# Kernel optimization log

Measured on AMD Instinct MI355X. Metric: run time of the kernel, lower is better.

## Reference

```python
import jax, jax.numpy as jnp
import numpy as np

B, NB, V1, V2, S, J, D, F = 32, 10, 3, 3, 2, 25, 3, 8
DIN = D * F          # 24
H1, H2 = 2 * DIN, 3 * DIN  # 48, 72
NFEAT, NCLASS = 256, 60
EPS = 1e-5


def _layernorm(h, g, b):
    m = jnp.mean(h, axis=-1, keepdims=True)
    v = jnp.mean(jnp.square(h - m), axis=-1, keepdims=True)
    return (h - m) * jax.lax.rsqrt(v + EPS) * g + b


def setup_inputs() -> dict:
    key = jax.random.key(0)
    ks = jax.random.split(key, 12)
    x = jax.random.normal(ks[0], (B, NB, V1, V2, S * J, D, F), dtype=jnp.float32)
    a = jax.random.uniform(ks[1], (J, J), dtype=jnp.float32)
    adj = a / jnp.sum(a, axis=1, keepdims=True)  # row-normalized dense adjacency
    sc = 0.05
    return {
        "x": x,
        "adj": adj,
        "W1": sc * jax.random.normal(ks[2], (DIN, H1), jnp.float32),
        "b1": jnp.zeros((H1,), jnp.float32),
        "g1": jnp.ones((H1,), jnp.float32),
        "be1": jnp.zeros((H1,), jnp.float32),
        "W2": sc * jax.random.normal(ks[3], (H1, H2), jnp.float32),
        "b2": jnp.zeros((H2,), jnp.float32),
        "g2": jnp.ones((H2,), jnp.float32),
        "be2": jnp.zeros((H2,), jnp.float32),
        "W3": sc * jax.random.normal(ks[4], (H2, NFEAT), jnp.float32),
        "b3": jnp.zeros((NFEAT,), jnp.float32),
        "g3": jnp.ones((NFEAT,), jnp.float32),
        "be3": jnp.zeros((NFEAT,), jnp.float32),
        "Wc": sc * jax.random.normal(ks[5], (J * NFEAT, NCLASS), jnp.float32),
        "bc": jnp.zeros((NCLASS,), jnp.float32),
        "batch_size": B,
        "degree": 4,
        "nclass": NCLASS,
        "alpha": 0.2,
    }


def _sgc_precompute(f0, adj, degree, alpha):
    # f0: [..., J, NFEAT]; repeated sparse-style propagation with accumulation
    def step(carry, _):
        f, acc = carry
        f = jnp.einsum('ij,...jf->...if', adj, f)
        acc = acc + (1.0 - alpha) * f + alpha * f0
        return (f, acc), None
    (_, acc), _ = jax.lax.scan(step, (f0, jnp.zeros_like(f0)), None, length=degree)
    return acc / degree


def reference(x, adj, W1, b1, g1, be1, W2, b2, g2, be2, W3, b3, g3, be3,
              Wc, bc, batch_size, degree, nclass, alpha):
    # split joints into (subject, joint) and flatten (D, F) per joint -> [B,NB,V1,V2,S,J,DIN]
    h = x.reshape(B, NB, V1, V2, S, J, DIN)
    h = jax.nn.relu(_layernorm(h @ W1 + b1, g1, be1))
    h = jax.nn.relu(_layernorm(h @ W2 + b2, g2, be2))
    h = _layernorm(h @ W3 + b3, g3, be3)            # dropout is identity in eval
    h = _sgc_precompute(h, adj, degree, alpha)       # [B,NB,V1,V2,S,J,NFEAT]
    vec = h.reshape(B, NB, V1, V2, S, J * NFEAT)
    logits = vec @ Wc + bc                            # [B,NB,V1,V2,S,NCLASS]
    block_mean = jnp.mean(logits, axis=4)             # mean over subjects
    pred = jnp.mean(block_mean, axis=(1, 2, 3))       # [B, NCLASS]
    return block_mean, pred
```

## Files before the change

### kernel.cpp

```cpp
#include <hip/hip_runtime.h>
#include <hip/hip_bf16.h>

typedef __hip_bfloat16 bf16t;
typedef _Float16 half_t;
typedef __attribute__((ext_vector_type(2))) _Float16 half2v;
typedef __attribute__((ext_vector_type(8))) _Float16 half8v;
typedef __attribute__((ext_vector_type(4))) float f32x4;
typedef unsigned int uint32;

#define BB   32
#define NC   60
#define NROW 2880
#define NFOLDB 1600
#define EPSF 1e-5f
#define ALPHA 0.2f
#define DEG  4

#define WS_M_OFF    256
#define WS_PW_OFF   4096
#define WS_W3BF_OFF 28672
#define WS_W2BF_OFF 77824
#define WS_W1BF_OFF 88064
#define WS_WCP_OFF  101376
#define WS_WCPF_OFF 869376
#define WS_PART_OFF 1688576
#define WS_GH3_OFF  7586816
#define WS_NEED     44450816ULL

#define P_W1  0
#define P_B1  1152
#define P_G1  1200
#define P_BE1 1248
#define P_W2  1296
#define P_B2  4752
#define P_G2  4824
#define P_BE2 4896
#define P_B3  4968
#define P_G3  5224
#define P_BE3 5480
#define P_BC  5736
#define P_TOT 5796
#define R_W3E (P_TOT+24576)
#define R_W2E (R_W3E+5120)
#define R_W1E (R_W2E+1536)
#define PREP_K1B 145

#define LB_H3L 0
#define LB_A1  12800
#define LB_CS  12800
#define LB_A2  22016
#define LB_H3H 22016
#define LB_STW 35328
#define LB_ST2 37376
#define LDS_FTOT 9472

__device__ __forceinline__ float ldin(const void* p, int i, int isbf){
  return isbf ? __bfloat162float(((const bf16t*)p)[i]) : ((const float*)p)[i];
}
__device__ __forceinline__ void stout(void* p, int i, int isbf, float v){
  if(isbf) ((bf16t*)p)[i] = __float2bfloat16(v);
  else     ((float*)p)[i] = v;
}
__device__ __forceinline__ half2v u2h2(uint32 u){
  half2v h; __builtin_memcpy(&h,&u,4); return h;
}
__device__ __forceinline__ uint32 pk2u(float a, float b){
  auto r = __builtin_amdgcn_cvt_pkrtz(a, b);
  uint32 u; __builtin_memcpy(&u,&r,4); return u;
}


__global__ void k_prep(const void* W1,const void* b1,const void* g1,const void* be1,
                       const void* W2,const void* b2,const void* g2,const void* be2,
                       const void* W3,const void* b3,const void* g3,const void* be3,
                       const void* bc, const void* x, const void* adj,
                       int* flagp, float* pw, float* M,
                       half_t* W3bf, half_t* W2bf, half_t* W1bf){
  __shared__ float A[625], Pp[625], Q[625], Ss[625];
  __shared__ int cnt;
  int t = threadIdx.x, bid = blockIdx.x;
  if(t==0) cnt = 0;
  __syncthreads();
  {
    const unsigned short* xb = (const unsigned short*)x;
    unsigned short u = xb[2*t];
    int e = (u>>7)&0xFF;
    if(e>=100 && e<=141) atomicAdd(&cnt,1);
  }
  __syncthreads();
  int isbf = (cnt>=160) ? 1 : 0;
  if(bid==0 && t==0) flagp[0] = isbf;

  if(bid < PREP_K1B){
    int o = bid*256 + t;
    if(o < P_TOT){
      const void* src; int loc;
      if      (o < P_B1 ) { src=W1;  loc=o;        }
      else if (o < P_G1 ) { src=b1;  loc=o-P_B1;   }
      else if (o < P_BE1) { src=g1;  loc=o-P_G1;   }
      else if (o < P_W2 ) { src=be1; loc=o-P_BE1;  }
      else if (o < P_B2 ) { src=W2;  loc=o-P_W2;   }
      else if (o < P_G2 ) { src=b2;  loc=o-P_B2;   }
      else if (o < P_BE2) { src=g2;  loc=o-P_G2;   }
      else if (o < P_B3 ) { src=be2; loc=o-P_BE2;  }
      else if (o < P_G3 ) { src=b3;  loc=o-P_B3;   }
      else if (o < P_BE3) { src=g3;  loc=o-P_G3;   }
      else if (o < P_BC ) { src=be3; loc=o-P_BE3;  }
      else                { src=bc;  loc=o-P_BC;   }
      pw[o] = ldin(src, loc, isbf);
    } else if(o < R_W3E){
      int o2 = o - P_TOT;
      int ct = o2/1536, rem = o2 - ct*1536;
      int kt = rem/512, rem2 = rem - kt*512;
      int l = rem2>>3, j = rem2&7;
      int k = kt*32 + ((l>>4)<<3) + j;
      int col = (ct<<4) + (l&15);
      float v = (k<72) ? ldin(W3, k*256+col, isbf) : 0.f;
      W3bf[o2] = (half_t)v;
    } else if(o < R_W2E){
      int o2 = o - R_W3E;
      int ct = o2/1024, rem = o2 - ct*1024;
      int kt = rem/512, rem2 = rem - kt*512;
      int l = rem2>>3, j = rem2&7;
      int k = kt*32 + ((l>>4)<<3) + j;
      int col = (ct<<4) + (l&15);
      float v = (k<48 && col<72) ? ldin(W2, k*72+col, isbf) : 0.f;
      W2bf[o2] = (half_t)v;
    } else if(o < R_W1E){
      int o2 = o - R_W2E;
      int ct = o2/512, rem2 = o2 - ct*512;
      int l = rem2>>3, j = rem2&7;
      int k = ((l>>4)<<3) + j;
      int col = (ct<<4) + (l&15);
      float v = (k<24) ? ldin(W1, k*48+col, isbf) : 0.f;
      W1bf[o2] = (half_t)v;
    }
  } else {
    for(int i=t;i<625;i+=256){ float a=ldin(adj,i,isbf); A[i]=a; Pp[i]=a; Ss[i]=a; }
    __syncthreads();
    for(int d=1; d<DEG; ++d){
      for(int o=t;o<625;o+=256){
        int i=o/25, j=o%25; float acc=0.f;
        for(int k=0;k<25;k++) acc += A[i*25+k]*Pp[k*25+j];
        Q[o]=acc;
      }
      __syncthreads();
      for(int o=t;o<625;o+=256){ Pp[o]=Q[o]; Ss[o]+=Q[o]; }
      __syncthreads();
    }
    const float coef = (1.0f-ALPHA)/(float)DEG;
    for(int o=t;o<625;o+=256){
      int i=o/25, j=o%25;
      M[o] = (i==j ? ALPHA : 0.0f) + coef*Ss[o];
    }
  }
}

__global__ __launch_bounds__(256,4) void k3_fast(const void* x, const float* pw,
                                              const half_t* W3bf_, const half_t* W2bf_,
                                              const half_t* W1bf_,
                                              const float* M, const void* Wc,
                                              half_t* Wcpf,
                                              const int* flagp, uint32* gH3d){
  __shared__ float sm[LDS_FTOT];
  char* smb = (char*)sm;
  half_t* H3L = (half_t*)(smb + LB_H3L);
  half_t* H3H = (half_t*)(smb + LB_H3H);
  half_t* A1h = (half_t*)(smb + LB_A1);
  half_t* A2h = (half_t*)(smb + LB_A2);
  half_t* XH  = A2h;
  float*  stw = (float*)(smb + LB_STW);
  float*  st2 = (float*)(smb + LB_ST2);
  uint32* A1w = (uint32*)A1h;
  const unsigned short* W3u = (const unsigned short*)W3bf_;
  const unsigned short* W2u = (const unsigned short*)W2bf_;
  const unsigned short* W1u = (const unsigned short*)W1bf_;

  int t = threadIdx.x, bid = blockIdx.x;
  int isbf = flagp[0];

  if(bid >= NROW){
    int o = (bid-NROW)*256 + t;
    int j = o&7, l = (o>>3)&63, nt = (o>>9)&3, kst = o>>11;
    int k = kst*32 + ((l>>4)<<3) + j;
    int c = nt*16 + (l&15);
    float acc = 0.f;
    if(c < 60){
      int jj = k>>8, f = k&255;
      for(int i=0;i<25;i++) acc += M[i*25+jj]*ldin(Wc, (i*256+f)*60 + c, isbf);
    }
    Wcpf[o] = (half_t)(0.5f*acc);
    return;
  }

  int l = t&63, w = t>>6, cb = l&15, g4 = l>>4;
  const float* b1=pw+P_B1;  const float* g1=pw+P_G1;  const float* be1=pw+P_BE1;
  const float* b2=pw+P_B2;  const float* g2=pw+P_G2;  const float* be2=pw+P_BE2;
  const float* b3=pw+P_B3;  const float* g3=pw+P_G3;  const float* be3=pw+P_BE3;

  for(int o=t;o<512;o+=256){ int r=o>>3, dc=24+(o&7); A1w[r*36+dc]=0; }
  {
    int xoff = bid*1200;
    for(int i=t;i<2560;i+=256){
      int r=i/40, c=i-(i/40)*40;
      float v = (r<50 && c<24) ? ldin(x, xoff + r*24+c, isbf) : 0.f;
      XH[i] = (half_t)v;
    }
  }
  __syncthreads();

  {
    f32x4 acc1[3];
    float g1v[3], be1v[3];
    #pragma unroll
    for(int ct=0;ct<3;ct++){
      int col = ct*16 + cb;
      float b = b1[col]; g1v[ct]=g1[col]; be1v[ct]=be1[col];
      acc1[ct][0]=b; acc1[ct][1]=b; acc1[ct][2]=b; acc1[ct][3]=b;
    }
    half8v a = *(const half8v*)(XH + (w*16 + cb)*40 + (g4<<3));
    #pragma unroll
    for(int ct=0;ct<3;ct++){
      half8v b = *(const half8v*)(W1u + (ct*64 + l)*8);
      acc1[ct] = __builtin_amdgcn_mfma_f32_16x16x32_f16(a, b, acc1[ct], 0,0,0);
    }
    __syncthreads();
    #pragma unroll
    for(int r=0;r<4;r++){
      float s1 = acc1[0][r]+acc1[1][r]+acc1[2][r];
      float s2 = acc1[0][r]*acc1[0][r]+acc1[1][r]*acc1[1][r]+acc1[2][r]*acc1[2][r];
      #pragma unroll
      for(int d=1;d<16;d<<=1){ s1+=__shfl_xor(s1,d,64); s2+=__shfl_xor(s2,d,64); }
      float m = s1*(1.f/48.f);
      float var = s2*(1.f/48.f)-m*m;
      float rs = rsqrtf(var+EPSF);
      int row = w*16 + (g4<<2) + r;
      #pragma unroll
      for(int ct=0;ct<3;ct++){
        float val = (acc1[ct][r]-m)*rs*g1v[ct]+be1v[ct];
        A1h[row*72 + ct*16 + cb] = (half_t)fmaxf(val,0.f);
      }
    }
  }
  __syncthreads();

  {
    f32x4 acc2[5];
    #pragma unroll
    for(int ct=0;ct<5;ct++){
      int col = ct*16 + cb;
      float b = (col<72) ? b2[col] : 0.f;
      acc2[ct][0]=b; acc2[ct][1]=b; acc2[ct][2]=b; acc2[ct][3]=b;
    }
    #pragma unroll
    for(int kt=0;kt<2;kt++){
      half8v a = *(const half8v*)(A1h + (w*16 + cb)*72 + kt*32 + (g4<<3));
      #pragma unroll
      for(int ct=0;ct<5;ct++){
        half8v b = *(const half8v*)(W2u + ((ct*2+kt)*64 + l)*8);
        acc2[ct] = __builtin_amdgcn_mfma_f32_16x16x32_f16(a, b, acc2[ct], 0,0,0);
      }
    }
    __syncthreads();
    int valid4 = (cb<8);
    #pragma unroll
    for(int r=0;r<4;r++){
      float s1 = acc2[0][r]+acc2[1][r]+acc2[2][r]+acc2[3][r] + (valid4?acc2[4][r]:0.f);
      float s2 = acc2[0][r]*acc2[0][r]+acc2[1][r]*acc2[1][r]
               + acc2[2][r]*acc2[2][r]+acc2[3][r]*acc2[3][r]
               + (valid4?acc2[4][r]*acc2[4][r]:0.f);
      #pragma unroll
      for(int d=1;d<16;d<<=1){ s1+=__shfl_xor(s1,d,64); s2+=__shfl_xor(s2,d,64); }
      float m = s1*(1.f/72.f);
      float var = s2*(1.f/72.f)-m*m;
      float rs = rsqrtf(var+EPSF);
      int grow = w*16 + (g4<<2) + r;
      #pragma unroll
      for(int ct=0;ct<5;ct++){
        int col = ct*16 + cb;
        if(ct<4 || valid4){
          float val = (acc2[ct][r]-m)*rs*g2[col]+be2[col];
          A2h[grow*104+col] = (half_t)fmaxf(val,0.f);
        }
      }
    }
    uint32* A2w = (uint32*)A2h;
    for(int o=l;o<192;o+=64){ int rr = w*16 + o/12, dc = 36 + (o - (o/12)*12); A2w[rr*52+dc]=0; }
  }
  __syncthreads();

  #pragma unroll 1
  for(int p=0;p<2;p++){
    f32x4 acc[2][4];
    #pragma unroll
    for(int nt=0;nt<4;nt++){
      float b3c = b3[w*64 + nt*16 + cb];
      #pragma unroll
      for(int m2=0;m2<2;m2++){ acc[m2][nt][0]=b3c; acc[m2][nt][1]=b3c; acc[m2][nt][2]=b3c; acc[m2][nt][3]=b3c; }
    }
    #pragma unroll
    for(int kt=0;kt<3;kt++){
      half8v a[2];
      #pragma unroll
      for(int m2=0;m2<2;m2++)
        a[m2] = *(const half8v*)(A2h + ((p*2+m2)*16+cb)*104 + kt*32 + (g4<<3));
      #pragma unroll
      for(int nt=0;nt<4;nt++){
        int ct = w*4 + nt;
        half8v b = *(const half8v*)(W3u + ((ct*3+kt)*64 + l)*8);
        #pragma unroll
        for(int m2=0;m2<2;m2++)
          acc[m2][nt] = __builtin_amdgcn_mfma_f32_16x16x32_f16(a[m2], b, acc[m2][nt], 0,0,0);
      }
    }
    __syncthreads();
    #pragma unroll
    for(int m2=0;m2<2;m2++){
      #pragma unroll
      for(int r=0;r<4;r++){
        int row = (p*2+m2)*16 + (g4<<2) + r;
        float s1 = acc[m2][0][r]+acc[m2][1][r]+acc[m2][2][r]+acc[m2][3][r];
        float s2 = acc[m2][0][r]*acc[m2][0][r]+acc[m2][1][r]*acc[m2][1][r]
                 + acc[m2][2][r]*acc[m2][2][r]+acc[m2][3][r]*acc[m2][3][r];
        #pragma unroll
        for(int d=1;d<16;d<<=1){ s1+=__shfl_xor(s1,d,64); s2+=__shfl_xor(s2,d,64); }
        if(cb==0){
          stw[row*8 + w*2]   = s1;
          stw[row*8 + w*2+1] = s2;
        }
        if(row<50){
          #pragma unroll
          for(int nt=0;nt<4;nt++){
            int col = w*64 + nt*16 + cb;
            if(row<25) H3L[row*256+col]      = (half_t)acc[m2][nt][r];
            else       H3H[(row-25)*256+col] = (half_t)acc[m2][nt][r];
          }
        }
      }
    }
  }
  __syncthreads();
  if(t<64){
    float S1 = stw[t*8+0]+stw[t*8+2]+stw[t*8+4]+stw[t*8+6];
    float S2 = stw[t*8+1]+stw[t*8+3]+stw[t*8+5]+stw[t*8+7];
    float m = S1*(1.f/256.f);
    float var = S2*(1.f/256.f)-m*m;
    st2[2*t]=m; st2[2*t+1]=rsqrtf(var+EPSF);
  }
  __syncthreads();
  {
    uint32* H3l32 = (uint32*)H3L;
    uint32* H3h32 = (uint32*)H3H;
    int cp = t & 127, ro = t>>7;
    float ga=g3[2*cp], gb=g3[2*cp+1], ba=be3[2*cp], bb=be3[2*cp+1];
    for(int r=ro; r<25; r+=2){
      uint32 lo = H3l32[r*128+cp], hi = H3h32[r*128+cp];
      float ml=st2[2*r], rl=st2[2*r+1];
      float mh=st2[2*(r+25)], rh=st2[2*(r+25)+1];
      half2v l2=u2h2(lo), h2=u2h2(hi);
      float v0 = ((float)l2[0]-ml)*rl*ga+ba + ((float)h2[0]-mh)*rh*ga+ba;
      float v1 = ((float)l2[1]-ml)*rl*gb+bb + ((float)h2[1]-mh)*rh*gb+bb;
      gH3d[(size_t)bid*3200 + r*128 + cp] = pk2u(v0, v1);
    }
  }
}

__global__ __launch_bounds__(256) void k5_gemm(const half_t* gH3, const half_t* Wcpf,
                                               float* part){
  int bx = blockIdx.x, ky = blockIdx.y;
  int t = threadIdx.x, l = t&63, w = t>>6, cb = l&15, g4 = l>>4;
  const unsigned short* H = (const unsigned short*)gH3;
  const unsigned short* W = (const unsigned short*)Wcpf;
  int base = bx*64 + w*16;
  f32x4 acc[4];
  #pragma unroll
  for(int nt=0;nt<4;nt++){ acc[nt][0]=0.f; acc[nt][1]=0.f; acc[nt][2]=0.f; acc[nt][3]=0.f; }
  int kst0 = ky*25;
  for(int ks=0;ks<25;ks++){
    int kst = kst0 + ks;
    half8v a = *(const half8v*)(H + (size_t)(base+cb)*6400 + kst*32 + (g4<<3));
    #pragma unroll
    for(int nt=0;nt<4;nt++){
      half8v b = *(const half8v*)(W + ((kst*4+nt)*64 + l)*8);
      acc[nt] = __builtin_amdgcn_mfma_f32_16x16x32_f16(a, b, acc[nt], 0,0,0);
    }
  }
  #pragma unroll
  for(int nt=0;nt<4;nt++){
    #pragma unroll
    for(int r=0;r<4;r++){
      int inst = base + (g4<<2) + r;
      part[((size_t)ky*NROW + inst)*64 + nt*16 + cb] = acc[nt][r];
    }
  }
}

__global__ void k6_out(const float* part, const float* pw, const int* flagp, void* out){
  __shared__ float bm[5400];
  int b = blockIdx.x, t = threadIdx.x;
  int isbf = flagp[0];
  for(int o=t;o<5400;o+=256){
    int li = o/60, c = o - li*60;
    int inst = b*90 + li;
    float v = pw[P_BC + c];
    #pragma unroll
    for(int ky=0;ky<8;ky++) v += part[((size_t)ky*NROW + inst)*64 + c];
    bm[o] = v;
    stout(out, inst*NC + c, isbf, v);
  }
  __syncthreads();
  if(t<NC){
    float a = 0.f;
    for(int r=0;r<90;r++) a += bm[r*60+t];
    stout(out, NROW*NC + b*NC + t, isbf, a*(1.f/90.f));
  }
}


__global__ void k0_prep(const void* x, const void* adj, int* flagp, float* M){
  __shared__ float A[625], P[625], Q[625], Ss[625];
  __shared__ int cnt, flg;
  int t = threadIdx.x;
  if(t==0) cnt = 0;
  __syncthreads();
  {
    const unsigned short* xb = (const unsigned short*)x;
    unsigned short u = xb[2*t];
    int e = (u>>7)&0xFF;
    if(e>=100 && e<=141) atomicAdd(&cnt,1);
  }
  __syncthreads();
  if(t==0){ flg = (cnt>=160)?1:0; flagp[0]=flg; }
  __syncthreads();
  int isbf = flg;
  for(int i=t;i<625;i+=256){ float a=ldin(adj,i,isbf); A[i]=a; P[i]=a; Ss[i]=a; }
  __syncthreads();
  for(int d=1; d<DEG; ++d){
    for(int o=t;o<625;o+=256){
      int i=o/25, j=o%25; float acc=0.f;
      for(int k=0;k<25;k++) acc += A[i*25+k]*P[k*25+j];
      Q[o]=acc;
    }
    __syncthreads();
    for(int o=t;o<625;o+=256){ P[o]=Q[o]; Ss[o]+=Q[o]; }
    __syncthreads();
  }
  const float coef = (1.0f-ALPHA)/(float)DEG;
  for(int o=t;o<625;o+=256){
    int i=o/25, j=o%25;
    M[o] = (i==j ? ALPHA : 0.0f) + coef*Ss[o];
  }
}

__global__ void k1_all(const void* W1,const void* b1,const void* g1,const void* be1,
                       const void* W2,const void* b2,const void* g2,const void* be2,
                       const void* W3,const void* b3,const void* g3,const void* be3,
                       const void* bc, const int* flagp,
                       float* pw, half_t* W3bf, half_t* W2bf, half_t* W1bf){
  int isbf = flagp[0];
  int o = blockIdx.x*256 + threadIdx.x;
  if(o < P_TOT){
    const void* src; int loc;
    if      (o < P_B1 ) { src=W1;  loc=o;        }
    else if (o < P_G1 ) { src=b1;  loc=o-P_B1;   }
    else if (o < P_BE1) { src=g1;  loc=o-P_G1;   }
    else if (o < P_W2 ) { src=be1; loc=o-P_BE1;  }
    else if (o < P_B2 ) { src=W2;  loc=o-P_W2;   }
    else if (o < P_G2 ) { src=b2;  loc=o-P_B2;   }
    else if (o < P_BE2) { src=g2;  loc=o-P_G2;   }
    else if (o < P_B3 ) { src=be2; loc=o-P_BE2;  }
    else if (o < P_G3 ) { src=b3;  loc=o-P_B3;   }
    else if (o < P_BE3) { src=g3;  loc=o-P_G3;   }
    else if (o < P_BC ) { src=be3; loc=o-P_BE3;  }
    else                { src=bc;  loc=o-P_BC;   }
    pw[o] = ldin(src, loc, isbf);
  } else if(o < R_W3E){
    int o2 = o - P_TOT;
    int ct = o2/1536, rem = o2 - ct*1536;
    int kt = rem/512, rem2 = rem - kt*512;
    int l = rem2>>3, j = rem2&7;
    int k = kt*32 + ((l>>4)<<3) + j;
    int col = (ct<<4) + (l&15);
    float v = (k<72) ? ldin(W3, k*256+col, isbf) : 0.f;
    W3bf[o2] = (half_t)v;
  } else if(o < R_W2E){
    int o2 = o - R_W3E;
    int ct = o2/1024, rem = o2 - ct*1024;
    int kt = rem/512, rem2 = rem - kt*512;
    int l = rem2>>3, j = rem2&7;
    int k = kt*32 + ((l>>4)<<3) + j;
    int col = (ct<<4) + (l&15);
    float v = (k<48 && col<72) ? ldin(W2, k*72+col, isbf) : 0.f;
    W2bf[o2] = (half_t)v;
  } else if(o < R_W1E){
    int o2 = o - R_W2E;
    int ct = o2/512, rem2 = o2 - ct*512;
    int l = rem2>>3, j = rem2&7;
    int k = ((l>>4)<<3) + j;
    int col = (ct<<4) + (l&15);
    float v = (k<24) ? ldin(W1, k*48+col, isbf) : 0.f;
    W1bf[o2] = (half_t)v;
  }
}

__global__ void k2_fold(const void* Wc, const float* M, const int* flagp, half_t* Wcp4){
  int isbf = flagp[0];
  int o = blockIdx.x*256 + threadIdx.x;
  if(o >= 384000) return;
  int grp = o>>4, hw = o&15;
  int kt = grp/15, cg = grp - kt*15;
  int p = hw>>3, cl = (hw>>1)&3, e = hw&1;
  int fl = kt*4 + 2*p + e;
  int j = fl>>8, f = fl&255;
  int c = cg*4 + cl;
  float acc = 0.f;
  for(int i=0;i<25;i++) acc += M[i*25+j]*ldin(Wc, (i*256+f)*60 + c, isbf);
  Wcp4[o] = (half_t)(0.5f*acc);
}

__global__ __launch_bounds__(256,4) void k3_fused(const void* x, const float* pw,
                                              const half_t* W3bf_, const half_t* W2bf_,
                                              const half_t* W1bf_,
                                              const unsigned short* Wcp4,
                                              const int* flagp, void* out){
  __shared__ float sm[LDS_FTOT];
  char* smb = (char*)sm;
  half_t* H3L = (half_t*)(smb + LB_H3L);
  half_t* H3H = (half_t*)(smb + LB_H3H);
  half_t* A1h = (half_t*)(smb + LB_A1);
  half_t* A2h = (half_t*)(smb + LB_A2);
  half_t* XH  = A2h;
  float*  stw = (float*)(smb + LB_STW);
  float*  st2 = (float*)(smb + LB_ST2);
  float*  cs  = (float*)(smb + LB_CS);
  uint32* A1w = (uint32*)A1h;
  const unsigned short* W3u = (const unsigned short*)W3bf_;
  const unsigned short* W2u = (const unsigned short*)W2bf_;
  const unsigned short* W1u = (const unsigned short*)W1bf_;

  int t = threadIdx.x, bid = blockIdx.x;
  int l = t&63, w = t>>6, cb = l&15, g4 = l>>4;
  int isbf = flagp[0];
  const float* b1=pw+P_B1;  const float* g1=pw+P_G1;  const float* be1=pw+P_BE1;
  const float* b2=pw+P_B2;  const float* g2=pw+P_G2;  const float* be2=pw+P_BE2;
  const float* b3=pw+P_B3;  const float* g3=pw+P_G3;  const float* be3=pw+P_BE3;
  const float* bc=pw+P_BC;

  for(int o=t;o<512;o+=256){ int r=o>>3, dc=24+(o&7); A1w[r*36+dc]=0; }
  {
    int xoff = bid*1200;
    for(int i=t;i<2560;i+=256){
      int r=i/40, c=i-(i/40)*40;
      float v = (r<50 && c<24) ? ldin(x, xoff + r*24+c, isbf) : 0.f;
      XH[i] = (half_t)v;
    }
  }
  __syncthreads();
  {
    f32x4 acc1[3];
    float g1v[3], be1v[3];
    #pragma unroll
    for(int ct=0;ct<3;ct++){
      int col = ct*16 + cb;
      float b = b1[col]; g1v[ct]=g1[col]; be1v[ct]=be1[col];
      acc1[ct][0]=b; acc1[ct][1]=b; acc1[ct][2]=b; acc1[ct][3]=b;
    }
    half8v a = *(const half8v*)(XH + (w*16 + cb)*40 + (g4<<3));
    #pragma unroll
    for(int ct=0;ct<3;ct++){
      half8v b = *(const half8v*)(W1u + (ct*64 + l)*8);
      acc1[ct] = __builtin_amdgcn_mfma_f32_16x16x32_f16(a, b, acc1[ct], 0,0,0);
    }
    __syncthreads();
    #pragma unroll
    for(int r=0;r<4;r++){
      float s1 = acc1[0][r]+acc1[1][r]+acc1[2][r];
      float s2 = acc1[0][r]*acc1[0][r]+acc1[1][r]*acc1[1][r]+acc1[2][r]*acc1[2][r];
      #pragma unroll
      for(int d=1;d<16;d<<=1){ s1+=__shfl_xor(s1,d,64); s2+=__shfl_xor(s2,d,64); }
      float m = s1*(1.f/48.f);
      float var = s2*(1.f/48.f)-m*m;
      float rs = rsqrtf(var+EPSF);
      int row = w*16 + (g4<<2) + r;
      #pragma unroll
      for(int ct=0;ct<3;ct++){
        float val = (acc1[ct][r]-m)*rs*g1v[ct]+be1v[ct];
        A1h[row*72 + ct*16 + cb] = (half_t)fmaxf(val,0.f);
      }
    }
  }
  __syncthreads();
  {
    f32x4 acc2[5];
    #pragma unroll
    for(int ct=0;ct<5;ct++){
      int col = ct*16 + cb;
      float b = (col<72) ? b2[col] : 0.f;
      acc2[ct][0]=b; acc2[ct][1]=b; acc2[ct][2]=b; acc2[ct][3]=b;
    }
    #pragma unroll
    for(int kt=0;kt<2;kt++){
      half8v a = *(const half8v*)(A1h + (w*16 + cb)*72 + kt*32 + (g4<<3));
      #pragma unroll
      for(int ct=0;ct<5;ct++){
        half8v b = *(const half8v*)(W2u + ((ct*2+kt)*64 + l)*8);
        acc2[ct] = __builtin_amdgcn_mfma_f32_16x16x32_f16(a, b, acc2[ct], 0,0,0);
      }
    }
    __syncthreads();
    int valid4 = (cb<8);
    #pragma unroll
    for(int r=0;r<4;r++){
      float s1 = acc2[0][r]+acc2[1][r]+acc2[2][r]+acc2[3][r] + (valid4?acc2[4][r]:0.f);
      float s2 = acc2[0][r]*acc2[0][r]+acc2[1][r]*acc2[1][r]
               + acc2[2][r]*acc2[2][r]+acc2[3][r]*acc2[3][r]
               + (valid4?acc2[4][r]*acc2[4][r]:0.f);
      #pragma unroll
      for(int d=1;d<16;d<<=1){ s1+=__shfl_xor(s1,d,64); s2+=__shfl_xor(s2,d,64); }
      float m = s1*(1.f/72.f);
      float var = s2*(1.f/72.f)-m*m;
      float rs = rsqrtf(var+EPSF);
      int grow = w*16 + (g4<<2) + r;
      #pragma unroll
      for(int ct=0;ct<5;ct++){
        int col = ct*16 + cb;
        if(ct<4 || valid4){
          float val = (acc2[ct][r]-m)*rs*g2[col]+be2[col];
          A2h[grow*104+col] = (half_t)fmaxf(val,0.f);
        }
      }
    }
    uint32* A2w = (uint32*)A2h;
    for(int o=l;o<192;o+=64){ int rr = w*16 + o/12, dc = 36 + (o - (o/12)*12); A2w[rr*52+dc]=0; }
  }
  __syncthreads();
  #pragma unroll 1
  for(int p=0;p<2;p++){
    f32x4 acc[2][4];
    #pragma unroll
    for(int nt=0;nt<4;nt++){
      float b3c = b3[w*64 + nt*16 + cb];
      #pragma unroll
      for(int m2=0;m2<2;m2++){ acc[m2][nt][0]=b3c; acc[m2][nt][1]=b3c; acc[m2][nt][2]=b3c; acc[m2][nt][3]=b3c; }
    }
    #pragma unroll
    for(int kt=0;kt<3;kt++){
      half8v a[2];
      #pragma unroll
      for(int m2=0;m2<2;m2++)
        a[m2] = *(const half8v*)(A2h + ((p*2+m2)*16+cb)*104 + kt*32 + (g4<<3));
      #pragma unroll
      for(int nt=0;nt<4;nt++){
        int ct = w*4 + nt;
        half8v b = *(const half8v*)(W3u + ((ct*3+kt)*64 + l)*8);
        #pragma unroll
        for(int m2=0;m2<2;m2++)
          acc[m2][nt] = __builtin_amdgcn_mfma_f32_16x16x32_f16(a[m2], b, acc[m2][nt], 0,0,0);
      }
    }
    __syncthreads();
    #pragma unroll
    for(int m2=0;m2<2;m2++){
      #pragma unroll
      for(int r=0;r<4;r++){
        int row = (p*2+m2)*16 + (g4<<2) + r;
        float s1 = acc[m2][0][r]+acc[m2][1][r]+acc[m2][2][r]+acc[m2][3][r];
        float s2 = acc[m2][0][r]*acc[m2][0][r]+acc[m2][1][r]*acc[m2][1][r]
                 + acc[m2][2][r]*acc[m2][2][r]+acc[m2][3][r]*acc[m2][3][r];
        #pragma unroll
        for(int d=1;d<16;d<<=1){ s1+=__shfl_xor(s1,d,64); s2+=__shfl_xor(s2,d,64); }
        if(cb==0){
          stw[row*8 + w*2]   = s1;
          stw[row*8 + w*2+1] = s2;
        }
        if(row<50){
          #pragma unroll
          for(int nt=0;nt<4;nt++){
            int col = w*64 + nt*16 + cb;
            if(row<25) H3L[row*256+col]      = (half_t)acc[m2][nt][r];
            else       H3H[(row-25)*256+col] = (half_t)acc[m2][nt][r];
          }
        }
      }
    }
  }
  __syncthreads();
  if(t<64){
    float S1 = stw[t*8+0]+stw[t*8+2]+stw[t*8+4]+stw[t*8+6];
    float S2 = stw[t*8+1]+stw[t*8+3]+stw[t*8+5]+stw[t*8+7];
    float m = S1*(1.f/256.f);
    float var = S2*(1.f/256.f)-m*m;
    st2[2*t]=m; st2[2*t+1]=rsqrtf(var+EPSF);
  }
  __syncthreads();
  {
    uint32* H3l32 = (uint32*)H3L;
    uint32* H3h32 = (uint32*)H3H;
    int cp = t & 127, ro = t>>7;
    float ga=g3[2*cp], gb=g3[2*cp+1], ba=be3[2*cp], bb=be3[2*cp+1];
    for(int r=ro; r<25; r+=2){
      uint32 lo = H3l32[r*128+cp], hi = H3h32[r*128+cp];
      float ml=st2[2*r], rl=st2[2*r+1];
      float mh=st2[2*(r+25)], rh=st2[2*(r+25)+1];
      half2v l2=u2h2(lo), h2=u2h2(hi);
      float v0 = ((float)l2[0]-ml)*rl*ga+ba + ((float)h2[0]-mh)*rh*ga+ba;
      float v1 = ((float)l2[1]-ml)*rl*gb+bb + ((float)h2[1]-mh)*rh*gb+bb;
      H3l32[r*128+cp] = pk2u(v0, v1);
    }
  }
  __syncthreads();
  {
    int cgc = (cb<15)?cb:14;
    int ktbase = w*400 + g4*100;
    const unsigned short* H3u = (const unsigned short*)H3L;
    float a0=0.f,a1=0.f,a2=0.f,a3=0.f;
    for(int i=0;i<100;i++){
      int kt = ktbase + i;
      uint2 hq = *(const uint2*)(H3u + kt*4);
      const uint4* qp = (const uint4*)(Wcp4 + (size_t)(kt*15+cgc)*16);
      uint4 wa = qp[0], wb = qp[1];
      half2v h01 = u2h2(hq.x), h23 = u2h2(hq.y);
      a0 = __builtin_amdgcn_fdot2(h01, u2h2(wa.x), a0, false);
      a0 = __builtin_amdgcn_fdot2(h23, u2h2(wb.x), a0, false);
      a1 = __builtin_amdgcn_fdot2(h01, u2h2(wa.y), a1, false);
      a1 = __builtin_amdgcn_fdot2(h23, u2h2(wb.y), a1, false);
      a2 = __builtin_amdgcn_fdot2(h01, u2h2(wa.z), a2, false);
      a2 = __builtin_amdgcn_fdot2(h23, u2h2(wb.z), a2, false);
      a3 = __builtin_amdgcn_fdot2(h01, u2h2(wa.w), a3, false);
      a3 = __builtin_amdgcn_fdot2(h23, u2h2(wb.w), a3, false);
    }
    a0 += __shfl_xor(a0,16,64); a0 += __shfl_xor(a0,32,64);
    a1 += __shfl_xor(a1,16,64); a1 += __shfl_xor(a1,32,64);
    a2 += __shfl_xor(a2,16,64); a2 += __shfl_xor(a2,32,64);
    a3 += __shfl_xor(a3,16,64); a3 += __shfl_xor(a3,32,64);
    if(l<15){
      cs[w*60 + l*4 + 0] = a0;
      cs[w*60 + l*4 + 1] = a1;
      cs[w*60 + l*4 + 2] = a2;
      cs[w*60 + l*4 + 3] = a3;
    }
  }
  __syncthreads();
  if(t<NC){
    float v = cs[t]+cs[60+t]+cs[120+t]+cs[180+t] + bc[t];
    stout(out, bid*NC+t, isbf, v);
  }
}

__global__ void k4_pred(const void* bm, const int* flagp, void* out){
  int b = blockIdx.x, t = threadIdx.x;
  int isbf = flagp[0];
  if(t<NC){
    float acc=0.f;
    for(int r=0;r<90;r++) acc += ldin(bm, (b*90+r)*NC+t, isbf);
    stout(out, NROW*NC + b*NC + t, isbf, acc*(1.f/90.f));
  }
}

extern "C" void kernel_launch(void* const* d_in, const int* in_sizes, int n_in,
                              void* d_out, int out_size, void* d_ws, size_t ws_size,
                              hipStream_t stream){
  const void* x   = d_in[0];
  const void* adj = d_in[1];
  char* ws = (char*)d_ws;
  int*     flagp = (int*)ws;
  float*   M     = (float*)(ws + WS_M_OFF);
  float*   pw    = (float*)(ws + WS_PW_OFF);
  half_t*  W3bf  = (half_t*)(ws + WS_W3BF_OFF);
  half_t*  W2bf  = (half_t*)(ws + WS_W2BF_OFF);
  half_t*  W1bf  = (half_t*)(ws + WS_W1BF_OFF);
  half_t*  Wcp4  = (half_t*)(ws + WS_WCP_OFF);
  half_t*  Wcpf  = (half_t*)(ws + WS_WCPF_OFF);
  float*   part  = (float*)(ws + WS_PART_OFF);
  half_t*  gH3   = (half_t*)(ws + WS_GH3_OFF);
  bool fast = (ws_size >= WS_NEED);

  if(fast){
    k_prep<<<PREP_K1B+1,256,0,stream>>>(d_in[2],d_in[3],d_in[4],d_in[5],
                                        d_in[6],d_in[7],d_in[8],d_in[9],
                                        d_in[10],d_in[11],d_in[12],d_in[13],
                                        d_in[15], x, adj,
                                        flagp, pw, M, W3bf, W2bf, W1bf);
    k3_fast<<<NROW+NFOLDB,256,0,stream>>>(x, pw, W3bf, W2bf, W1bf,
                                          M, d_in[14], Wcpf, flagp, (uint32*)gH3);
    dim3 g5(45,8);
    k5_gemm<<<g5,256,0,stream>>>(gH3, Wcpf, part);
    k6_out<<<BB,256,0,stream>>>(part, pw, flagp, d_out);
  } else {
    k0_prep<<<1,256,0,stream>>>(x, adj, flagp, M);
    k1_all<<<(R_W1E+255)/256,256,0,stream>>>(d_in[2],d_in[3],d_in[4],d_in[5],
                                             d_in[6],d_in[7],d_in[8],d_in[9],
                                             d_in[10],d_in[11],d_in[12],d_in[13],
                                             d_in[15], flagp, pw, W3bf, W2bf, W1bf);
    k2_fold<<<1500,256,0,stream>>>(d_in[14], M, flagp, Wcp4);
    k3_fused<<<NROW,256,0,stream>>>(x, pw, W3bf, W2bf, W1bf,
                                    (const unsigned short*)Wcp4, flagp, d_out);
    k4_pred<<<BB,64,0,stream>>>(d_out, flagp, d_out);
  }
}
```

Measured before the change: 100.7 us.

## Load x directly into MFMA fragments, drop barriers, hoist W3 fragments

The first-layer A operand is now read straight from global memory into registers, rather than staged through LDS, which removes the staging loop and its block barrier. Two more __syncthreads are dropped because each wave only reads the A1/A2 rows it wrote itself, and A2 no longer aliases the x staging buffer. The W3 B-fragments and b3 bias are loaded once into registers before the two-pass loop instead of being reloaded each pass. The trade-offs are less coalesced per-lane global loads of x and about 48 extra VGPRs, which could reduce occupancy under the 256,4 launch bounds.

```diff
diff --git a/kernel.cpp b/kernel.cpp
--- a/kernel.cpp
+++ b/kernel.cpp
@@ -168,7 +168,6 @@
   half_t* H3H = (half_t*)(smb + LB_H3H);
   half_t* A1h = (half_t*)(smb + LB_A1);
   half_t* A2h = (half_t*)(smb + LB_A2);
-  half_t* XH  = A2h;
   float*  stw = (float*)(smb + LB_STW);
   float*  st2 = (float*)(smb + LB_ST2);
   uint32* A1w = (uint32*)A1h;
@@ -199,15 +198,6 @@
   const float* b3=pw+P_B3;  const float* g3=pw+P_G3;  const float* be3=pw+P_BE3;
 
   for(int o=t;o<512;o+=256){ int r=o>>3, dc=24+(o&7); A1w[r*36+dc]=0; }
-  {
-    int xoff = bid*1200;
-    for(int i=t;i<2560;i+=256){
-      int r=i/40, c=i-(i/40)*40;
-      float v = (r<50 && c<24) ? ldin(x, xoff + r*24+c, isbf) : 0.f;
-      XH[i] = (half_t)v;
-    }
-  }
-  __syncthreads();
 
   {
     f32x4 acc1[3];
@@ -218,7 +208,16 @@
       float b = b1[col]; g1v[ct]=g1[col]; be1v[ct]=be1[col];
       acc1[ct][0]=b; acc1[ct][1]=b; acc1[ct][2]=b; acc1[ct][3]=b;
     }
-    half8v a = *(const half8v*)(XH + (w*16 + cb)*40 + (g4<<3));
+    int row = w*16 + cb;
+    half8v a;
+    if(g4 < 3 && row < 50){
+      int base = bid*1200 + row*24 + g4*8;
+      #pragma unroll
+      for(int j=0;j<8;j++) a[j] = (half_t)ldin(x, base+j, isbf);
+    } else {
+      #pragma unroll
+      for(int j=0;j<8;j++) a[j] = (half_t)0.f;
+    }
     #pragma unroll
     for(int ct=0;ct<3;ct++){
       half8v b = *(const half8v*)(W1u + (ct*64 + l)*8);
@@ -234,15 +233,14 @@
       float m = s1*(1.f/48.f);
       float var = s2*(1.f/48.f)-m*m;
       float rs = rsqrtf(var+EPSF);
-      int row = w*16 + (g4<<2) + r;
+      int rw = w*16 + (g4<<2) + r;
       #pragma unroll
       for(int ct=0;ct<3;ct++){
         float val = (acc1[ct][r]-m)*rs*g1v[ct]+be1v[ct];
-        A1h[row*72 + ct*16 + cb] = (half_t)fmaxf(val,0.f);
-      }
-    }
-  }
-  __syncthreads();
+        A1h[rw*72 + ct*16 + cb] = (half_t)fmaxf(val,0.f);
+      }
+    }
+  }
 
   {
     f32x4 acc2[5];
@@ -261,7 +259,6 @@
         acc2[ct] = __builtin_amdgcn_mfma_f32_16x16x32_f16(a, b, acc2[ct], 0,0,0);
       }
     }
-    __syncthreads();
     int valid4 = (cb<8);
     #pragma unroll
     for(int r=0;r<4;r++){
@@ -289,14 +286,24 @@
   }
   __syncthreads();
 
+  half8v bfr[12];
+  #pragma unroll
+  for(int kt=0;kt<3;kt++){
+    #pragma unroll
+    for(int nt=0;nt<4;nt++)
+      bfr[kt*4+nt] = *(const half8v*)(W3u + (((w*4+nt)*3+kt)*64 + l)*8);
+  }
+  float b3v[4];
+  #pragma unroll
+  for(int nt=0;nt<4;nt++) b3v[nt] = b3[w*64 + nt*16 + cb];
+
   #pragma unroll 1
   for(int p=0;p<2;p++){
     f32x4 acc[2][4];
     #pragma unroll
     for(int nt=0;nt<4;nt++){
-      float b3c = b3[w*64 + nt*16 + cb];
-      #pragma unroll
-      for(int m2=0;m2<2;m2++){ acc[m2][nt][0]=b3c; acc[m2][nt][1]=b3c; acc[m2][nt][2]=b3c; acc[m2][nt][3]=b3c; }
+      #pragma unroll
+      for(int m2=0;m2<2;m2++){ acc[m2][nt][0]=b3v[nt]; acc[m2][nt][1]=b3v[nt]; acc[m2][nt][2]=b3v[nt]; acc[m2][nt][3]=b3v[nt]; }
     }
     #pragma unroll
     for(int kt=0;kt<3;kt++){
@@ -306,11 +313,9 @@
         a[m2] = *(const half8v*)(A2h + ((p*2+m2)*16+cb)*104 + kt*32 + (g4<<3));
       #pragma unroll
       for(int nt=0;nt<4;nt++){
-        int ct = w*4 + nt;
-        half8v b = *(const half8v*)(W3u + ((ct*3+kt)*64 + l)*8);
         #pragma unroll
         for(int m2=0;m2<2;m2++)
-          acc[m2][nt] = __builtin_amdgcn_mfma_f32_16x16x32_f16(a[m2], b, acc[m2][nt], 0,0,0);
+          acc[m2][nt] = __builtin_amdgcn_mfma_f32_16x16x32_f16(a[m2], bfr[kt*4+nt], acc[m2][nt], 0,0,0);
       }
     }
     __syncthreads();
```

New measurement: 96.01 us (median of 2 runs). 4.6% less time.
